# Optimization experiments

Measured on AMD Instinct MI355X. Metric: run time of the kernel, lower is better.

## Reference

```python
import jax, jax.numpy as jnp
import numpy as np

N, F, H = 4096, 256, 4

def setup_inputs() -> dict:
    key = jax.random.key(0)
    kx, kw, kb = jax.random.split(key, 3)
    x = jax.random.normal(kx, (N, F), dtype=jnp.float32)
    # per-head Linear(2F -> 1): weight [H, 2F], bias [H]
    lim = 1.0 / np.sqrt(2 * F)
    W = jax.random.uniform(kw, (H, 2 * F), minval=-lim, maxval=lim, dtype=jnp.float32)
    b = jax.random.uniform(kb, (H,), minval=-lim, maxval=lim, dtype=jnp.float32)
    return {"x": x, "W": W, "b": b}

def reference(x, W, b):
    n, f = x.shape
    # concat(x_i, x_j) @ w^T == x_i @ w1 + x_j @ w2  (separable score, same math)
    W1, W2 = W[:, :f], W[:, f:]            # [H,F] each
    s_i = x @ W1.T                          # [N,H] contribution of row node i
    s_j = x @ W2.T                          # [N,H] contribution of col node j
    # logits[h,i,j] = s_i[i,h] + s_j[j,h] + b[h]
    logits = s_i.T[:, :, None] + s_j.T[:, None, :] + b[:, None, None]  # [H,N,N]
    attn = jax.nn.softmax(logits, axis=2)   # softmax over neighbors j
    out_heads = jnp.einsum('hij,jf->hif', attn, x)  # [H,N,F]
    avg = jnp.mean(out_heads, axis=0)       # [N,F]
    return jax.nn.leaky_relu(avg, negative_slope=0.2)
```

## Files before the change

kernel.cpp:

```cpp
#include <hip/hip_runtime.h>


#define NROWS 4096
#define FDIM  256
#define HHEADS 4
#define ROWS_PER_BLK 64
#define PAD 260


__global__ __launch_bounds__(256) void k1_scores(const float* __restrict__ x,
                                                 const float* __restrict__ W,
                                                 float* __restrict__ u,
                                                 float* __restrict__ Z) {
    __shared__ float x_lds[ROWS_PER_BLK * PAD];
    __shared__ float w_lds[FDIM * HHEADS];
    __shared__ float e_lds[ROWS_PER_BLK * HHEADS];

    const int t = threadIdx.x;
    const int row0 = blockIdx.x * ROWS_PER_BLK;

    for (int i = t; i < FDIM * HHEADS; i += 256) {
        int h = i >> 8, c = i & 255;
        w_lds[c * 4 + h] = W[h * (2 * FDIM) + FDIM + c];
    }
    for (int i = t; i < ROWS_PER_BLK * (FDIM / 4); i += 256) {
        int r = i >> 6, c4 = i & 63;
        float4 v = ((const float4*)x)[(size_t)(row0 + r) * (FDIM / 4) + c4];
        *(float4*)&x_lds[r * PAD + c4 * 4] = v;
    }
    __syncthreads();

    {
        int r = t >> 2, h = t & 3;
        const float* xr = &x_lds[r * PAD];
        float acc = 0.f;
        #pragma unroll 8
        for (int c = 0; c < FDIM; ++c)
            acc = fmaf(xr[c], w_lds[c * 4 + h], acc);
        e_lds[r * 4 + h] = __expf(acc);
    }
    __syncthreads();

    if (t < HHEADS) {
        float z = 0.f;
        for (int r = 0; r < ROWS_PER_BLK; ++r) z += e_lds[r * 4 + t];
        atomicAdd(&Z[t], z);
    }

    float a0 = 0.f, a1 = 0.f, a2 = 0.f, a3 = 0.f;
    for (int r = 0; r < ROWS_PER_BLK; ++r) {
        float xv = x_lds[r * PAD + t];
        float4 e4 = *(const float4*)&e_lds[r * 4];
        a0 = fmaf(e4.x, xv, a0);
        a1 = fmaf(e4.y, xv, a1);
        a2 = fmaf(e4.z, xv, a2);
        a3 = fmaf(e4.w, xv, a3);
    }
    atomicAdd(&u[0 * FDIM + t], a0);
    atomicAdd(&u[1 * FDIM + t], a1);
    atomicAdd(&u[2 * FDIM + t], a2);
    atomicAdd(&u[3 * FDIM + t], a3);
}

__global__ __launch_bounds__(256) void k2_out(const float* __restrict__ u,
                                              const float* __restrict__ Z,
                                              float* __restrict__ out) {
    __shared__ float v_lds[FDIM];
    const int t = threadIdx.x;
    {
        float z0 = Z[0], z1 = Z[1], z2 = Z[2], z3 = Z[3];
        float val = 0.25f * (u[t] / z0 + u[FDIM + t] / z1 +
                             u[2 * FDIM + t] / z2 + u[3 * FDIM + t] / z3);
        v_lds[t] = val > 0.f ? val : 0.2f * val;
    }
    __syncthreads();

    const int row0 = blockIdx.x * 8;
    const int c4 = t & 63;
    const int sub = t >> 6;
    float4 val4 = *(const float4*)&v_lds[c4 * 4];
    float4* out4 = (float4*)out;
    out4[(size_t)(row0 + sub) * (FDIM / 4) + c4] = val4;
    out4[(size_t)(row0 + sub + 4) * (FDIM / 4) + c4] = val4;
}

extern "C" void kernel_launch(void* const* d_in, const int* in_sizes, int n_in,
                              void* d_out, int out_size, void* d_ws, size_t ws_size,
                              hipStream_t stream) {
    const float* x = (const float*)d_in[0];
    const float* W = (const float*)d_in[1];
    float* u = (float*)d_ws;
    float* Z = u + HHEADS * FDIM;
    float* out = (float*)d_out;

    hipMemsetAsync(d_ws, 0, (HHEADS * FDIM + HHEADS) * sizeof(float), stream);
    k1_scores<<<NROWS / ROWS_PER_BLK, 256, 0, stream>>>(x, W, u, Z);
    k2_out<<<NROWS / 8, 256, 0, stream>>>(u, Z, out);
}
```

Before: 72.30 us.

## Replace atomics and memset with per-block partials reduced in output kernel

The first kernel now writes per-block partial sums of the weighted features and softmax denominators to workspace instead of atomically adding into a zeroed buffer, which removes the memset launch and the atomic contention. The second kernel has each block redundantly reduce all 64 partials before broadcasting the row to 64 output rows, using fewer, larger blocks. The weight layout in shared memory is also changed to allow float4 dot products. In exchange, every output block rereads 256KB of partials, and the second kernel runs with only 64 blocks.

```diff
diff --git a/kernel.cpp b/kernel.cpp
--- a/kernel.cpp
+++ b/kernel.cpp
@@ -4,26 +4,27 @@
 #define NROWS 4096
 #define FDIM  256
 #define HHEADS 4
-#define ROWS_PER_BLK 64
+#define RPB 64
+#define NB1 (NROWS / RPB)
 #define PAD 260
 
 
-__global__ __launch_bounds__(256) void k1_scores(const float* __restrict__ x,
-                                                 const float* __restrict__ W,
-                                                 float* __restrict__ u,
-                                                 float* __restrict__ Z) {
-    __shared__ float x_lds[ROWS_PER_BLK * PAD];
-    __shared__ float w_lds[FDIM * HHEADS];
-    __shared__ float e_lds[ROWS_PER_BLK * HHEADS];
+__global__ __launch_bounds__(256) void k1_partials(const float* __restrict__ x,
+                                                   const float* __restrict__ W,
+                                                   float* __restrict__ partU,
+                                                   float* __restrict__ partZ) {
+    __shared__ float x_lds[RPB * PAD];
+    __shared__ float w_lds[HHEADS * FDIM];
+    __shared__ float e_lds[RPB * HHEADS];
 
     const int t = threadIdx.x;
-    const int row0 = blockIdx.x * ROWS_PER_BLK;
+    const int row0 = blockIdx.x * RPB;
 
-    for (int i = t; i < FDIM * HHEADS; i += 256) {
+    for (int i = t; i < HHEADS * FDIM; i += 256) {
         int h = i >> 8, c = i & 255;
-        w_lds[c * 4 + h] = W[h * (2 * FDIM) + FDIM + c];
+        w_lds[i] = W[h * (2 * FDIM) + FDIM + c];
     }
-    for (int i = t; i < ROWS_PER_BLK * (FDIM / 4); i += 256) {
+    for (int i = t; i < RPB * (FDIM / 4); i += 256) {
         int r = i >> 6, c4 = i & 63;
         float4 v = ((const float4*)x)[(size_t)(row0 + r) * (FDIM / 4) + c4];
         *(float4*)&x_lds[r * PAD + c4 * 4] = v;
@@ -32,23 +33,26 @@
 
     {
         int r = t >> 2, h = t & 3;
-        const float* xr = &x_lds[r * PAD];
+        const float4* xr = (const float4*)&x_lds[r * PAD];
+        const float4* wr = (const float4*)&w_lds[h * FDIM];
         float acc = 0.f;
         #pragma unroll 8
-        for (int c = 0; c < FDIM; ++c)
-            acc = fmaf(xr[c], w_lds[c * 4 + h], acc);
+        for (int c = 0; c < FDIM / 4; ++c) {
+            float4 a = xr[c], b = wr[c];
+            acc = fmaf(a.x, b.x, fmaf(a.y, b.y, fmaf(a.z, b.z, fmaf(a.w, b.w, acc))));
+        }
         e_lds[r * 4 + h] = __expf(acc);
     }
     __syncthreads();
 
     if (t < HHEADS) {
         float z = 0.f;
-        for (int r = 0; r < ROWS_PER_BLK; ++r) z += e_lds[r * 4 + t];
-        atomicAdd(&Z[t], z);
+        for (int r = 0; r < RPB; ++r) z += e_lds[r * 4 + t];
+        partZ[blockIdx.x * HHEADS + t] = z;
     }
 
     float a0 = 0.f, a1 = 0.f, a2 = 0.f, a3 = 0.f;
-    for (int r = 0; r < ROWS_PER_BLK; ++r) {
+    for (int r = 0; r < RPB; ++r) {
         float xv = x_lds[r * PAD + t];
         float4 e4 = *(const float4*)&e_lds[r * 4];
         a0 = fmaf(e4.x, xv, a0);
@@ -56,32 +60,48 @@
         a2 = fmaf(e4.z, xv, a2);
         a3 = fmaf(e4.w, xv, a3);
     }
-    atomicAdd(&u[0 * FDIM + t], a0);
-    atomicAdd(&u[1 * FDIM + t], a1);
-    atomicAdd(&u[2 * FDIM + t], a2);
-    atomicAdd(&u[3 * FDIM + t], a3);
+    float* pu = partU + (size_t)blockIdx.x * (HHEADS * FDIM);
+    pu[0 * FDIM + t] = a0;
+    pu[1 * FDIM + t] = a1;
+    pu[2 * FDIM + t] = a2;
+    pu[3 * FDIM + t] = a3;
 }
 
-__global__ __launch_bounds__(256) void k2_out(const float* __restrict__ u,
-                                              const float* __restrict__ Z,
+__global__ __launch_bounds__(256) void k2_out(const float* __restrict__ partU,
+                                              const float* __restrict__ partZ,
                                               float* __restrict__ out) {
     __shared__ float v_lds[FDIM];
+    __shared__ float zinv[HHEADS];
     const int t = threadIdx.x;
-    {
-        float z0 = Z[0], z1 = Z[1], z2 = Z[2], z3 = Z[3];
-        float val = 0.25f * (u[t] / z0 + u[FDIM + t] / z1 +
-                             u[2 * FDIM + t] / z2 + u[3 * FDIM + t] / z3);
-        v_lds[t] = val > 0.f ? val : 0.2f * val;
+
+    if (t < HHEADS) {
+        float z = 0.f;
+        for (int b = 0; b < NB1; ++b) z += partZ[b * HHEADS + t];
+        zinv[t] = 1.0f / z;
+    }
+
+    float u0 = 0.f, u1 = 0.f, u2 = 0.f, u3 = 0.f;
+    for (int b = 0; b < NB1; ++b) {
+        const float* p = partU + (size_t)b * (HHEADS * FDIM);
+        u0 += p[0 * FDIM + t];
+        u1 += p[1 * FDIM + t];
+        u2 += p[2 * FDIM + t];
+        u3 += p[3 * FDIM + t];
     }
     __syncthreads();
 
-    const int row0 = blockIdx.x * 8;
-    const int c4 = t & 63;
-    const int sub = t >> 6;
-    float4 val4 = *(const float4*)&v_lds[c4 * 4];
+    float val = 0.25f * (u0 * zinv[0] + u1 * zinv[1] + u2 * zinv[2] + u3 * zinv[3]);
+    v_lds[t] = val > 0.f ? val : 0.2f * val;
+    __syncthreads();
+
+    const int row0 = blockIdx.x * 64;
     float4* out4 = (float4*)out;
-    out4[(size_t)(row0 + sub) * (FDIM / 4) + c4] = val4;
-    out4[(size_t)(row0 + sub + 4) * (FDIM / 4) + c4] = val4;
+    #pragma unroll
+    for (int i = 0; i < 16; ++i) {
+        int idx = t + i * 256;
+        int r = idx >> 6, c4 = idx & 63;
+        out4[(size_t)(row0 + r) * (FDIM / 4) + c4] = *(const float4*)&v_lds[c4 * 4];
+    }
 }
 
 extern "C" void kernel_launch(void* const* d_in, const int* in_sizes, int n_in,
@@ -89,11 +109,10 @@
                               hipStream_t stream) {
     const float* x = (const float*)d_in[0];
     const float* W = (const float*)d_in[1];
-    float* u = (float*)d_ws;
-    float* Z = u + HHEADS * FDIM;
+    float* partU = (float*)d_ws;
+    float* partZ = partU + (size_t)NB1 * HHEADS * FDIM;
     float* out = (float*)d_out;
 
-    hipMemsetAsync(d_ws, 0, (HHEADS * FDIM + HHEADS) * sizeof(float), stream);
-    k1_scores<<<NROWS / ROWS_PER_BLK, 256, 0, stream>>>(x, W, u, Z);
-    k2_out<<<NROWS / 8, 256, 0, stream>>>(u, Z, out);
+    k1_partials<<<NB1, 256, 0, stream>>>(x, W, partU, partZ);
+    k2_out<<<NROWS / 64, 256, 0, stream>>>(partU, partZ, out);
 }
```

Result: slower. 74.34 us (+2.8%).
